# Kernel tuning notes

Hardware: AMD Instinct MI355X
Metric: run time of the kernel (lower is better)

Reference implementation:

```python
import jax, jax.numpy as jnp
import numpy as np

TAU = 0.2  # args.gumble_tau


def _segment_softmax(vals, seg, num_seg):
    # torch.sparse.softmax(dim=1): softmax over the nonzero entries of each row
    m = jax.ops.segment_max(vals, seg, num_segments=num_seg)
    e = jnp.exp(vals - m[seg])
    s = jax.ops.segment_sum(e, seg, num_segments=num_seg)
    return e / s[seg]


def _masked_attention(q_embed, k_embed, Wq, bq, Wk, bk, rows, cols, noise, num_rows):
    # Q = self.Q(q_embed); K = self.K(k_embed)
    Q = q_embed @ Wq + bq            # [Nq, H]
    K = k_embed @ Wk + bk            # [Nk, H]
    # sparse_dense_mul(adj, Q @ K.T) -> only gather edge entries (same math)
    w = jnp.sum(Q[rows] * K[cols], axis=-1)   # [E]
    g = jnp.log(-jnp.log(noise))              # gumble_G = log(-log(rand))
    z = (w - g) / TAU
    return _segment_softmax(z, rows, num_rows)


def setup_inputs() -> dict:
    key = jax.random.key(0)
    ks = jax.random.split(key, 10)
    U, I, D, H, E = 50000, 25000, 256, 128, 1600000
    inp = {
        "user_embed": jax.random.normal(ks[0], (U, D), jnp.float32),
        "item_embed": jax.random.normal(ks[1], (I, D), jnp.float32),
        "Wq": jax.random.normal(ks[2], (D, H), jnp.float32) * 0.05,
        "bq": jax.random.normal(ks[3], (H,), jnp.float32) * 0.05,
        "Wk": jax.random.normal(ks[4], (D, H), jnp.float32) * 0.05,
        "bk": jax.random.normal(ks[5], (H,), jnp.float32) * 0.05,
        "ui_rows": jax.random.randint(ks[6], (E,), 0, U, jnp.int32),
        "ui_cols": jax.random.randint(ks[7], (E,), 0, I, jnp.int32),
        "noise_ui": jax.random.uniform(ks[8], (E,), jnp.float32, 1e-6, 1.0),
        "noise_iu": jax.random.uniform(ks[9], (E,), jnp.float32, 1e-6, 1.0),
    }
    return inp


def reference(user_embed, item_embed, Wq, bq, Wk, bk, ui_rows, ui_cols, noise_ui, noise_iu):
    U = user_embed.shape[0]
    I = item_embed.shape[0]
    # M_ui: rows = users, softmax over items per user
    vals_ui = _masked_attention(user_embed, item_embed, Wq, bq, Wk, bk,
                                ui_rows, ui_cols, noise_ui, U)
    # M_iu: transposed adjacency, rows = items, same Q/K layers
    vals_iu = _masked_attention(item_embed, user_embed, Wq, bq, Wk, bk,
                                ui_cols, ui_rows, noise_iu, I)
    # mask values = cat([M_ui.values(), M_iu.values()])
    return jnp.concatenate([vals_ui, vals_iu])
```

## Files before the change

kernel.cpp:

```cpp
#include <hip/hip_runtime.h>
#include <hip/hip_fp16.h>
#include <math.h>

#define TAU_INV 5.0f
#define LOG2E   1.4426950408889634f

typedef _Float16 half2v __attribute__((ext_vector_type(2)));
typedef _Float16 f16x8  __attribute__((ext_vector_type(8)));
typedef float    f32x4  __attribute__((ext_vector_type(4)));

__device__ __forceinline__ float fast_exp2(float x) { return __builtin_amdgcn_exp2f(x); }
__device__ __forceinline__ float fast_log2(float x) { return __builtin_amdgcn_logf(x); }

__device__ __forceinline__ double exp_double(float z) {
    float y = z * LOG2E;
    float n = rintf(y);
    float r = y - n;
    float f = fast_exp2(r);
    long long e = (long long)n + 1023;
    if (e < 1)    e = 1;
    if (e > 2046) e = 2046;
    double scale = __longlong_as_double(e << 52);
    return (double)f * scale;
}

__device__ __forceinline__ float log2_of_double(double v) {
    unsigned long long b = __double_as_longlong(v);
    int ex = (int)((b >> 52) & 0x7FFULL) - 1023;
    double m = __longlong_as_double((b & 0xFFFFFFFFFFFFFULL) | 0x3FF0000000000000ULL);
    return (float)ex + fast_log2((float)m);
}

__global__ __launch_bounds__(256) void convert_w(
    const float* __restrict__ Wq, const float* __restrict__ Wk,
    _Float16* __restrict__ Wt_hi, _Float16* __restrict__ Wt_lo)
{
    int t = blockIdx.x * 256 + threadIdx.x;
    int n = t >> 8;
    int k = t & 255;
    float x = (n < 128) ? Wq[k * 128 + n] : Wk[k * 128 + (n - 128)];
    _Float16 hi = (_Float16)x;
    _Float16 lo = (_Float16)(x - (float)hi);
    Wt_hi[n * 256 + k] = hi;
    Wt_lo[n * 256 + k] = lo;
}

__global__ __launch_bounds__(256) void gemm_qk_mfma(
    const float* __restrict__ Xu, const float* __restrict__ Xi,
    const _Float16* __restrict__ Wt_hi, const _Float16* __restrict__ Wt_lo,
    const float* __restrict__ bq, const float* __restrict__ bk,
    __half* __restrict__ QK, int U, int I)
{
    __shared__ _Float16 Ah[64][72];
    __shared__ _Float16 Al[64][72];

    const int tid  = threadIdx.x;
    const int row0 = blockIdx.x * 64;
    const int wv   = tid >> 6;
    const int l    = tid & 63;
    const int lr   = l & 15;
    const int kc   = l >> 4;
    const int n0   = wv * 64;
    const int NT   = U + I;

    f32x4 acc[4][4];
#pragma unroll
    for (int i = 0; i < 4; ++i)
#pragma unroll
        for (int j = 0; j < 4; ++j)
            acc[i][j] = (f32x4){0.f, 0.f, 0.f, 0.f};

    const int sr = tid >> 2;
    const int sk = (tid & 3) * 16;
    const float* Xrow = nullptr;
    {
        int gr = row0 + sr;
        if (gr < U)       Xrow = &Xu[(size_t)gr * 256];
        else if (gr < NT) Xrow = &Xi[(size_t)(gr - U) * 256];
    }

    for (int k0 = 0; k0 < 256; k0 += 64) {
        {
            float x[16];
            if (Xrow) {
                float4 v0 = *(const float4*)&Xrow[k0 + sk + 0];
                float4 v1 = *(const float4*)&Xrow[k0 + sk + 4];
                float4 v2 = *(const float4*)&Xrow[k0 + sk + 8];
                float4 v3 = *(const float4*)&Xrow[k0 + sk + 12];
                x[0]=v0.x; x[1]=v0.y; x[2]=v0.z; x[3]=v0.w;
                x[4]=v1.x; x[5]=v1.y; x[6]=v1.z; x[7]=v1.w;
                x[8]=v2.x; x[9]=v2.y; x[10]=v2.z; x[11]=v2.w;
                x[12]=v3.x; x[13]=v3.y; x[14]=v3.z; x[15]=v3.w;
            } else {
#pragma unroll
                for (int q = 0; q < 16; ++q) x[q] = 0.f;
            }
            _Float16 hi[16], lo[16];
#pragma unroll
            for (int q = 0; q < 16; ++q) {
                hi[q] = (_Float16)x[q];
                lo[q] = (_Float16)(x[q] - (float)hi[q]);
            }
            *(f16x8*)&Ah[sr][sk]     = *(const f16x8*)&hi[0];
            *(f16x8*)&Ah[sr][sk + 8] = *(const f16x8*)&hi[8];
            *(f16x8*)&Al[sr][sk]     = *(const f16x8*)&lo[0];
            *(f16x8*)&Al[sr][sk + 8] = *(const f16x8*)&lo[8];
        }
        __syncthreads();

#pragma unroll
        for (int kk = 0; kk < 2; ++kk) {
            const int kof = kk * 32 + kc * 8;
            f16x8 ah[4], al[4];
#pragma unroll
            for (int i = 0; i < 4; ++i) {
                ah[i] = *(const f16x8*)&Ah[i * 16 + lr][kof];
                al[i] = *(const f16x8*)&Al[i * 16 + lr][kof];
            }
#pragma unroll
            for (int j = 0; j < 4; ++j) {
                const size_t wo = (size_t)(n0 + j * 16 + lr) * 256 + k0 + kof;
                f16x8 bh = *(const f16x8*)&Wt_hi[wo];
                f16x8 bl = *(const f16x8*)&Wt_lo[wo];
#pragma unroll
                for (int i = 0; i < 4; ++i) {
                    acc[i][j] = __builtin_amdgcn_mfma_f32_16x16x32_f16(ah[i], bh, acc[i][j], 0, 0, 0);
                    acc[i][j] = __builtin_amdgcn_mfma_f32_16x16x32_f16(al[i], bh, acc[i][j], 0, 0, 0);
                    acc[i][j] = __builtin_amdgcn_mfma_f32_16x16x32_f16(ah[i], bl, acc[i][j], 0, 0, 0);
                }
            }
        }
        __syncthreads();
    }

    float bias[4];
#pragma unroll
    for (int j = 0; j < 4; ++j) {
        int col = n0 + j * 16 + lr;
        bias[j] = (col < 128) ? bq[col] : bk[col - 128];
    }
#pragma unroll
    for (int i = 0; i < 4; ++i) {
#pragma unroll
        for (int q = 0; q < 4; ++q) {
            int gr = row0 + i * 16 + kc * 4 + q;
            if (gr < NT) {
#pragma unroll
                for (int j = 0; j < 4; ++j) {
                    int col = n0 + j * 16 + lr;
                    QK[(size_t)gr * 256 + col] = __float2half_rn(acc[i][j][q] + bias[j]);
                }
            }
        }
    }
}

__global__ __launch_bounds__(256) void edge_w_both(
    const __half* __restrict__ QK,
    const int* __restrict__ rows, const int* __restrict__ cols,
    const float* __restrict__ noise_ui, const float* __restrict__ noise_iu,
    float* __restrict__ out, double* __restrict__ seg_sumd, int U, int E)
{
    const int gtid = blockIdx.x * 256 + threadIdx.x;
    const int eid  = gtid >> 3;
    if (eid >= E) return;
    const int hl = threadIdx.x & 7;

    const int r = __builtin_nontemporal_load(&rows[eid]);
    const int c = __builtin_nontemporal_load(&cols[eid]);
    const __half* urow = QK + (size_t)r * 256;
    const __half* irow = QK + (size_t)(U + c) * 256;

    const uint4 qu0 = *(const uint4*)(urow + hl * 16);
    const uint4 qu1 = *(const uint4*)(urow + hl * 16 + 8);
    const uint4 ku0 = *(const uint4*)(urow + 128 + hl * 16);
    const uint4 ku1 = *(const uint4*)(urow + 128 + hl * 16 + 8);
    const uint4 qi0 = *(const uint4*)(irow + hl * 16);
    const uint4 qi1 = *(const uint4*)(irow + hl * 16 + 8);
    const uint4 ki0 = *(const uint4*)(irow + 128 + hl * 16);
    const uint4 ki1 = *(const uint4*)(irow + 128 + hl * 16 + 8);

    float d0 = 0.0f, d1 = 0.0f;
    {
        const half2v* a0 = (const half2v*)&qu0;
        const half2v* b0 = (const half2v*)&ki0;
        const half2v* a1 = (const half2v*)&qi0;
        const half2v* b1 = (const half2v*)&ku0;
#pragma unroll
        for (int t = 0; t < 4; ++t) {
            d0 = __builtin_amdgcn_fdot2(a0[t], b0[t], d0, false);
            d1 = __builtin_amdgcn_fdot2(a1[t], b1[t], d1, false);
        }
        const half2v* a0b = (const half2v*)&qu1;
        const half2v* b0b = (const half2v*)&ki1;
        const half2v* a1b = (const half2v*)&qi1;
        const half2v* b1b = (const half2v*)&ku1;
#pragma unroll
        for (int t = 0; t < 4; ++t) {
            d0 = __builtin_amdgcn_fdot2(a0b[t], b0b[t], d0, false);
            d1 = __builtin_amdgcn_fdot2(a1b[t], b1b[t], d1, false);
        }
    }
    d0 += __shfl_xor(d0, 4);  d1 += __shfl_xor(d1, 4);
    d0 += __shfl_xor(d0, 2);  d1 += __shfl_xor(d1, 2);
    d0 += __shfl_xor(d0, 1);  d1 += __shfl_xor(d1, 1);

    if (hl < 2) {
        const int g  = hl;
        const float d  = g ? d1 : d0;
        const float nz = g ? __builtin_nontemporal_load(&noise_iu[eid])
                           : __builtin_nontemporal_load(&noise_ui[eid]);
        const float zz = (d - __logf(-__logf(nz))) * TAU_INV;
        const int s  = g ? (U + c) : r;
        __builtin_nontemporal_store(zz, &out[(size_t)g * E + eid]);
        atomicAdd(&seg_sumd[s], exp_double(zz));
    }
}

__global__ void edge_norm2v(float* __restrict__ z,
                            const int* __restrict__ rows, const int* __restrict__ cols,
                            const double* __restrict__ seg_sumd, int U, int E)
{
    int p = blockIdx.x * blockDim.x + threadIdx.x;
    int i = p * 2;
    if (i >= 2 * E) return;
    const bool iu  = (i >= E);
    const int base = iu ? (i - E) : i;
    const int off  = iu ? U : 0;
    const int* idx = iu ? cols : rows;
    int2 rc   = *(const int2*)&idx[base];
    float2 zz = *(const float2*)&z[i];
    float l0 = log2_of_double(seg_sumd[off + rc.x]);
    float l1 = log2_of_double(seg_sumd[off + rc.y]);
    float o0 = fast_exp2(zz.x * LOG2E - l0);
    float o1 = fast_exp2(zz.y * LOG2E - l1);
    *(float2*)&z[i] = make_float2(o0, o1);
}

__global__ void edge_norm2(float* __restrict__ z,
                           const int* __restrict__ rows, const int* __restrict__ cols,
                           const double* __restrict__ seg_sumd, int U, int E)
{
    int i = blockIdx.x * blockDim.x + threadIdx.x;
    if (i >= 2 * E) return;
    int s = (i < E) ? rows[i] : (U + cols[i - E]);
    float l = log2_of_double(seg_sumd[s]);
    z[i] = fast_exp2(z[i] * LOG2E - l);
}

extern "C" void kernel_launch(void* const* d_in, const int* in_sizes, int n_in,
                              void* d_out, int out_size, void* d_ws, size_t ws_size,
                              hipStream_t stream)
{
    const float* user_embed = (const float*)d_in[0];
    const float* item_embed = (const float*)d_in[1];
    const float* Wq = (const float*)d_in[2];
    const float* bq = (const float*)d_in[3];
    const float* Wk = (const float*)d_in[4];
    const float* bk = (const float*)d_in[5];
    const int* ui_rows    = (const int*)d_in[6];
    const int* ui_cols    = (const int*)d_in[7];
    const float* noise_ui = (const float*)d_in[8];
    const float* noise_iu = (const float*)d_in[9];

    const int H = in_sizes[3];
    const int D = in_sizes[2] / H;
    const int U = in_sizes[0] / D;
    const int I = in_sizes[1] / D;
    const int E = in_sizes[6];

    const int nseg = U + I;

    char* wsc = (char*)d_ws;
    __half* QK = (__half*)wsc;          wsc += (size_t)nseg * 256 * sizeof(__half);
    double* seg_sumd = (double*)wsc;    wsc += (size_t)nseg * sizeof(double);
    _Float16* Wt_hi = (_Float16*)wsc;   wsc += (size_t)256 * 256 * sizeof(_Float16);
    _Float16* Wt_lo = (_Float16*)wsc;   wsc += (size_t)256 * 256 * sizeof(_Float16);

    float* out = (float*)d_out;

    hipMemsetAsync(seg_sumd, 0, (size_t)nseg * sizeof(double), stream);

    convert_w<<<256, 256, 0, stream>>>(Wq, Wk, Wt_hi, Wt_lo);

    const int gblocks = (nseg + 63) / 64;
    gemm_qk_mfma<<<gblocks, 256, 0, stream>>>(user_embed, item_embed,
                                              Wt_hi, Wt_lo, bq, bk, QK, U, I);

    const int eblocks = (int)(((long long)E * 8 + 255) / 256);
    edge_w_both<<<eblocks, 256, 0, stream>>>(QK, ui_rows, ui_cols,
                                             noise_ui, noise_iu,
                                             out, seg_sumd, U, E);

    if ((E & 1) == 0) {
        const int vblocks = (E + 255) / 256;
        edge_norm2v<<<vblocks, 256, 0, stream>>>(out, ui_rows, ui_cols,
                                                 seg_sumd, U, E);
    } else {
        const int sblocks = (2 * E + 255) / 256;
        edge_norm2<<<sblocks, 256, 0, stream>>>(out, ui_rows, ui_cols,
                                                seg_sumd, U, E);
    }
}
```

Before: 439.0 us.

## Prefetch next X tile into registers and XOR-swizzle LDS in QK GEMM

The QK projection GEMM now loads the next 64-wide K slice of the embedding rows into registers with nontemporal loads while the current slice is being multiplied, so global latency overlaps with MFMA work. The shared-memory tiles drop their padding and use an XOR swizzle on 8-element chunks to avoid bank conflicts. Weight fragments for all four column tiles are loaded before the A fragments to give the scheduler more independent loads. This raises register pressure, and the GEMM is likely a minor part of the total time next to the edge kernels.

```diff
diff --git a/kernel.cpp b/kernel.cpp
--- a/kernel.cpp
+++ b/kernel.cpp
@@ -8,6 +8,7 @@
 typedef _Float16 half2v __attribute__((ext_vector_type(2)));
 typedef _Float16 f16x8  __attribute__((ext_vector_type(8)));
 typedef float    f32x4  __attribute__((ext_vector_type(4)));
+typedef float    fv4    __attribute__((ext_vector_type(4)));
 
 __device__ __forceinline__ float fast_exp2(float x) { return __builtin_amdgcn_exp2f(x); }
 __device__ __forceinline__ float fast_log2(float x) { return __builtin_amdgcn_logf(x); }
@@ -51,8 +52,8 @@
     const float* __restrict__ bq, const float* __restrict__ bk,
     __half* __restrict__ QK, int U, int I)
 {
-    __shared__ _Float16 Ah[64][72];
-    __shared__ _Float16 Al[64][72];
+    __shared__ _Float16 Ah[64][64];
+    __shared__ _Float16 Al[64][64];
 
     const int tid  = threadIdx.x;
     const int row0 = blockIdx.x * 64;
@@ -71,62 +72,78 @@
             acc[i][j] = (f32x4){0.f, 0.f, 0.f, 0.f};
 
     const int sr = tid >> 2;
-    const int sk = (tid & 3) * 16;
+    const int sc = (tid & 3) * 2;
     const float* Xrow = nullptr;
     {
         int gr = row0 + sr;
         if (gr < U)       Xrow = &Xu[(size_t)gr * 256];
         else if (gr < NT) Xrow = &Xi[(size_t)(gr - U) * 256];
     }
-
-    for (int k0 = 0; k0 < 256; k0 += 64) {
+    const int swz = sr & 7;
+    const int w0  = (sc ^ swz) * 8;
+    const int w1  = ((sc + 1) ^ swz) * 8;
+
+    fv4 nxa, nxb, nxc, nxd;
+    if (Xrow) {
+        const float* p = Xrow + sc * 8;
+        nxa = __builtin_nontemporal_load((const fv4*)(p + 0));
+        nxb = __builtin_nontemporal_load((const fv4*)(p + 4));
+        nxc = __builtin_nontemporal_load((const fv4*)(p + 8));
+        nxd = __builtin_nontemporal_load((const fv4*)(p + 12));
+    } else {
+        nxa = nxb = nxc = nxd = (fv4){0.f, 0.f, 0.f, 0.f};
+    }
+
+    for (int k0s = 0; k0s < 4; ++k0s) {
+        const int k0 = k0s * 64;
         {
-            float x[16];
-            if (Xrow) {
-                float4 v0 = *(const float4*)&Xrow[k0 + sk + 0];
-                float4 v1 = *(const float4*)&Xrow[k0 + sk + 4];
-                float4 v2 = *(const float4*)&Xrow[k0 + sk + 8];
-                float4 v3 = *(const float4*)&Xrow[k0 + sk + 12];
-                x[0]=v0.x; x[1]=v0.y; x[2]=v0.z; x[3]=v0.w;
-                x[4]=v1.x; x[5]=v1.y; x[6]=v1.z; x[7]=v1.w;
-                x[8]=v2.x; x[9]=v2.y; x[10]=v2.z; x[11]=v2.w;
-                x[12]=v3.x; x[13]=v3.y; x[14]=v3.z; x[15]=v3.w;
-            } else {
-#pragma unroll
-                for (int q = 0; q < 16; ++q) x[q] = 0.f;
-            }
+            float x[16] = {nxa.x, nxa.y, nxa.z, nxa.w,  nxb.x, nxb.y, nxb.z, nxb.w,
+                           nxc.x, nxc.y, nxc.z, nxc.w,  nxd.x, nxd.y, nxd.z, nxd.w};
             _Float16 hi[16], lo[16];
 #pragma unroll
             for (int q = 0; q < 16; ++q) {
                 hi[q] = (_Float16)x[q];
                 lo[q] = (_Float16)(x[q] - (float)hi[q]);
             }
-            *(f16x8*)&Ah[sr][sk]     = *(const f16x8*)&hi[0];
-            *(f16x8*)&Ah[sr][sk + 8] = *(const f16x8*)&hi[8];
-            *(f16x8*)&Al[sr][sk]     = *(const f16x8*)&lo[0];
-            *(f16x8*)&Al[sr][sk + 8] = *(const f16x8*)&lo[8];
+            *(f16x8*)&Ah[sr][w0] = *(const f16x8*)&hi[0];
+            *(f16x8*)&Ah[sr][w1] = *(const f16x8*)&hi[8];
+            *(f16x8*)&Al[sr][w0] = *(const f16x8*)&lo[0];
+            *(f16x8*)&Al[sr][w1] = *(const f16x8*)&lo[8];
         }
         __syncthreads();
 
+        if (Xrow && k0s < 3) {
+            const float* p = Xrow + (k0 + 64) + sc * 8;
+            nxa = __builtin_nontemporal_load((const fv4*)(p + 0));
+            nxb = __builtin_nontemporal_load((const fv4*)(p + 4));
+            nxc = __builtin_nontemporal_load((const fv4*)(p + 8));
+            nxd = __builtin_nontemporal_load((const fv4*)(p + 12));
+        }
+
 #pragma unroll
         for (int kk = 0; kk < 2; ++kk) {
-            const int kof = kk * 32 + kc * 8;
+            f16x8 bh[4], bl[4];
+#pragma unroll
+            for (int j = 0; j < 4; ++j) {
+                const size_t wo = (size_t)(n0 + j * 16 + lr) * 256 + k0 + kk * 32 + kc * 8;
+                bh[j] = *(const f16x8*)&Wt_hi[wo];
+                bl[j] = *(const f16x8*)&Wt_lo[wo];
+            }
             f16x8 ah[4], al[4];
 #pragma unroll
             for (int i = 0; i < 4; ++i) {
-                ah[i] = *(const f16x8*)&Ah[i * 16 + lr][kof];
-                al[i] = *(const f16x8*)&Al[i * 16 + lr][kof];
+                const int row = i * 16 + lr;
+                const int ch  = ((kk * 4 + kc) ^ (row & 7)) * 8;
+                ah[i] = *(const f16x8*)&Ah[row][ch];
+                al[i] = *(const f16x8*)&Al[row][ch];
             }
 #pragma unroll
             for (int j = 0; j < 4; ++j) {
-                const size_t wo = (size_t)(n0 + j * 16 + lr) * 256 + k0 + kof;
-                f16x8 bh = *(const f16x8*)&Wt_hi[wo];
-                f16x8 bl = *(const f16x8*)&Wt_lo[wo];
 #pragma unroll
                 for (int i = 0; i < 4; ++i) {
-                    acc[i][j] = __builtin_amdgcn_mfma_f32_16x16x32_f16(ah[i], bh, acc[i][j], 0, 0, 0);
-                    acc[i][j] = __builtin_amdgcn_mfma_f32_16x16x32_f16(al[i], bh, acc[i][j], 0, 0, 0);
-                    acc[i][j] = __builtin_amdgcn_mfma_f32_16x16x32_f16(ah[i], bl, acc[i][j], 0, 0, 0);
+                    acc[i][j] = __builtin_amdgcn_mfma_f32_16x16x32_f16(ah[i], bh[j], acc[i][j], 0, 0, 0);
+                    acc[i][j] = __builtin_amdgcn_mfma_f32_16x16x32_f16(al[i], bh[j], acc[i][j], 0, 0, 0);
+                    acc[i][j] = __builtin_amdgcn_mfma_f32_16x16x32_f16(ah[i], bl[j], acc[i][j], 0, 0, 0);
                 }
             }
         }
@@ -279,7 +296,7 @@
 
     float* out = (float*)d_out;
 
-    hipMemsetAsync(seg_sumd, 0, (size_t)nseg * sizeof(double), stream);
+    (void)hipMemsetAsync(seg_sumd, 0, (size_t)nseg * sizeof(double), stream);
 
     convert_w<<<256, 256, 0, stream>>>(Wq, Wk, Wt_hi, Wt_lo);
 
```

Result: no change. 445.9 us (+1.6%).
